# Kernel optimization log

Measured on AMD Instinct MI355X. Metric: run time of the kernel, lower is better.

Reference implementation:

```python
import math
import jax, jax.numpy as jnp
import numpy as np

NUM_HEADS = 12
NUM_LANDMARKS = 32

def iterative_inv(mat, n_iter=6):
    # mat: [B, H, m, m] row-stochastic kernel; Newton-Schulz pseudo-inverse
    m = mat.shape[-1]
    I = jnp.eye(m, dtype=mat.dtype)
    K = mat
    # 'else' branch: per-(B,H) normalization by max column sum
    denom = jnp.max(jnp.sum(K, axis=-2), axis=-1)[..., None, None]
    V = jnp.swapaxes(K, -1, -2) / denom
    for _ in range(n_iter):
        KV = jnp.matmul(K, V)
        V = jnp.matmul(0.25 * V, 13.0 * I - jnp.matmul(KV, 15.0 * I - jnp.matmul(KV, 7.0 * I - KV)))
    return V

def setup_inputs() -> dict:
    key = jax.random.key(0)
    k1, k2, k3 = jax.random.split(key, 3)
    B, N, C = 8, 2048, 768
    x = jax.random.normal(k1, (B, N, C), dtype=jnp.float32)
    w_qkv = jax.random.normal(k2, (C, 3 * C), dtype=jnp.float32) * (1.0 / math.sqrt(C))
    w_proj = jax.random.normal(k3, (C, C), dtype=jnp.float32) * (1.0 / math.sqrt(C))
    b_proj = jnp.zeros((C,), dtype=jnp.float32)
    return {"x": x, "w_qkv": w_qkv, "w_proj": w_proj, "b_proj": b_proj}

def reference(x, w_qkv, w_proj, b_proj):
    B, N, C = x.shape
    H = NUM_HEADS
    d = C // H
    m = NUM_LANDMARKS
    qkv = (x @ w_qkv).reshape(B, N, 3, H, d).transpose(2, 0, 3, 1, 4)  # [3,B,H,N,d]
    Q, K, V = qkv[0], qkv[1], qkv[2]
    scale = 1.0 / math.sqrt(math.sqrt(d))
    Q = Q * scale
    K = K * scale
    # landmark pooling: mean over contiguous chunks of size N//m
    Q_l = Q.reshape(B, H, m, N // m, d).mean(axis=-2)  # [B,H,m,d]
    K_l = K.reshape(B, H, m, N // m, d).mean(axis=-2)
    kernel_1 = jax.nn.softmax(jnp.einsum('bhnd,bhmd->bhnm', Q, K_l), axis=-1)   # [B,H,N,m]
    kernel_2 = jax.nn.softmax(jnp.einsum('bhmd,bhkd->bhmk', Q_l, K_l), axis=-1) # [B,H,m,m]
    kernel_3 = jax.nn.softmax(jnp.einsum('bhmd,bhnd->bhmn', Q_l, K), axis=-1)   # [B,H,m,N]
    X = jnp.matmul(jnp.matmul(kernel_1, iterative_inv(kernel_2)), jnp.matmul(kernel_3, V))  # [B,H,N,d]
    X = X.transpose(0, 2, 1, 3).reshape(B, N, C)
    return X @ w_proj + b_proj
```

## Files before the change

kernel.cpp:

```cpp
#include <hip/hip_runtime.h>
#include <hip/hip_bf16.h>

typedef __hip_bfloat16 bf16;
typedef __attribute__((ext_vector_type(8))) __bf16 bf16x8;
typedef __attribute__((ext_vector_type(4))) float f32x4;

#define NB 8
#define SEQ 2048
#define CH 768
#define NH 12
#define HD 64
#define NL 32
#define BHT (NB*NH)
#define TOK (NB*SEQ)
#define QK_SCALE 0.35355339059327379f

#define BAR() __builtin_amdgcn_s_barrier()
#define WLGKM0() __asm__ __volatile__("s_waitcnt lgkmcnt(0)" ::: "memory")
#define WVM(n) __asm__ __volatile__("s_waitcnt vmcnt(" #n ")" ::: "memory")

__device__ __forceinline__ void async_ld16(const bf16* g, bf16* l) {
    unsigned loff = (unsigned)__builtin_amdgcn_readfirstlane((int)(unsigned)(uintptr_t)l);
    __builtin_amdgcn_global_load_lds(
        (const __attribute__((address_space(1))) unsigned*)(uintptr_t)g,
        (__attribute__((address_space(3))) unsigned*)(uintptr_t)loff, 16, 0, 0);
}

__global__ void convert_x(const float* __restrict__ x, bf16* __restrict__ xb) {
    size_t i = ((size_t)blockIdx.x * 256 + threadIdx.x) * 8;
    float4 a = *reinterpret_cast<const float4*>(x + i);
    float4 b = *reinterpret_cast<const float4*>(x + i + 4);
    alignas(16) bf16 tmp[8];
    tmp[0] = __float2bfloat16(a.x); tmp[1] = __float2bfloat16(a.y);
    tmp[2] = __float2bfloat16(a.z); tmp[3] = __float2bfloat16(a.w);
    tmp[4] = __float2bfloat16(b.x); tmp[5] = __float2bfloat16(b.y);
    tmp[6] = __float2bfloat16(b.z); tmp[7] = __float2bfloat16(b.w);
    *reinterpret_cast<uint4*>(xb + i) = *reinterpret_cast<const uint4*>(tmp);
}

__global__ void transpose_f32(const float* __restrict__ in, bf16* __restrict__ outp,
                              int Hrows, int Wcols) {
    __shared__ float tile[32][33];
    int bx = blockIdx.x * 32, by = blockIdx.y * 32;
    int tx = threadIdx.x, ty = threadIdx.y;
    for (int i = 0; i < 32; i += 8)
        tile[ty + i][tx] = in[(size_t)(by + ty + i) * Wcols + bx + tx];
    __syncthreads();
    for (int i = 0; i < 32; i += 8)
        outp[(size_t)(bx + ty + i) * Hrows + by + tx] = __float2bfloat16(tile[tx][ty + i]);
}

template <int EPI>
__global__ __launch_bounds__(512, 2) void gemm_bt(
    const bf16* __restrict__ A, const bf16* __restrict__ Bt,
    int Nout, int Kdim,
    bf16* __restrict__ q, bf16* __restrict__ k, bf16* __restrict__ vt,
    float* __restrict__ Ql, float* __restrict__ Kl,
    float* __restrict__ outp, const float* __restrict__ bias_f) {
    __shared__ __align__(16) bf16 As[2][256 * 64];
    __shared__ __align__(16) bf16 Bs[2][192 * 64];
    const int t = threadIdx.x;
    const int wave = t >> 6, lane = t & 63;
    const int quad = lane >> 4, l15 = lane & 15;
    const int wr = wave >> 2, wc = wave & 3;

    int p = blockIdx.y * gridDim.x + blockIdx.x;
    int xcd = p & 7, j = p >> 3;
    int gx = gridDim.x;
    int bn = j % gx;
    int bm = (j / gx) * 8 + xcd;
    const int bm0 = bm * 256;
    const int bn0 = bn * 192;

    const int T = Kdim >> 6;

    const int srow = t >> 3;
    const int scol = (((t & 7) ^ (srow & 7)) << 3);
    const bf16* Abase = A + (size_t)(bm0 + srow) * Kdim + scol;
    const bf16* Bbase = Bt + (size_t)(bn0 + srow) * Kdim + scol;

    auto stA = [&](int kt, int c) {
        async_ld16(Abase + (size_t)(c * 64) * Kdim + kt * 64,
                   &As[kt & 1][c * 4096 + t * 8]);
    };
    auto stB = [&](int kt, int c) {
        async_ld16(Bbase + (size_t)(c * 64) * Kdim + kt * 64,
                   &Bs[kt & 1][c * 4096 + t * 8]);
    };

    const int swk[2] = { (quad ^ (l15 & 7)) << 3, ((4 + quad) ^ (l15 & 7)) << 3 };
    const bf16* arow = &As[0][(wr * 128 + l15) * 64];
    const bf16* brow = &Bs[0][(wc * 48 + l15) * 64];

    f32x4 acc[8][3];
    const f32x4 zero4 = {0.f, 0.f, 0.f, 0.f};
    #pragma unroll
    for (int i = 0; i < 8; i++)
        #pragma unroll
        for (int jj = 0; jj < 3; jj++) acc[i][jj] = zero4;

    stA(0, 0); stA(0, 2); stB(0, 0); stB(0, 1); stB(0, 2); stA(0, 1); stA(0, 3);
    WVM(2);
    BAR();

    bf16x8 a[4][2], b[3][2];
    #pragma unroll 2
    for (int kt = 0; kt < T; kt++) {
        const int cur = kt & 1;
        const bool nxt = (kt + 1 < T);
        const bf16* ab = arow + cur * 16384;
        const bf16* bb = brow + cur * 12288;

        #pragma unroll
        for (int mi = 0; mi < 4; mi++)
            #pragma unroll
            for (int kk = 0; kk < 2; kk++)
                a[mi][kk] = *reinterpret_cast<const bf16x8*>(ab + mi * 1024 + swk[kk]);
        #pragma unroll
        for (int ni = 0; ni < 2; ni++)
            #pragma unroll
            for (int kk = 0; kk < 2; kk++)
                b[ni][kk] = *reinterpret_cast<const bf16x8*>(bb + ni * 1024 + swk[kk]);
        if (nxt) { stA(kt + 1, 0); stA(kt + 1, 2); }
        BAR(); WLGKM0();
        __builtin_amdgcn_s_setprio(1);
        #pragma unroll
        for (int mi = 0; mi < 4; mi++)
            #pragma unroll
            for (int ni = 0; ni < 2; ni++)
                #pragma unroll
                for (int kk = 0; kk < 2; kk++)
                    acc[mi][ni] = __builtin_amdgcn_mfma_f32_16x16x32_bf16(a[mi][kk], b[ni][kk], acc[mi][ni], 0, 0, 0);
        __builtin_amdgcn_s_setprio(0);
        BAR();

        #pragma unroll
        for (int kk = 0; kk < 2; kk++)
            b[2][kk] = *reinterpret_cast<const bf16x8*>(bb + 2 * 1024 + swk[kk]);
        if (nxt) { stB(kt + 1, 0); stB(kt + 1, 1); }
        BAR(); WLGKM0();
        __builtin_amdgcn_s_setprio(1);
        #pragma unroll
        for (int mi = 0; mi < 4; mi++)
            #pragma unroll
            for (int kk = 0; kk < 2; kk++)
                acc[mi][2] = __builtin_amdgcn_mfma_f32_16x16x32_bf16(a[mi][kk], b[2][kk], acc[mi][2], 0, 0, 0);
        __builtin_amdgcn_s_setprio(0);
        if (nxt) { WVM(4); } else { WVM(0); }
        BAR();

        #pragma unroll
        for (int mi = 0; mi < 4; mi++)
            #pragma unroll
            for (int kk = 0; kk < 2; kk++)
                a[mi][kk] = *reinterpret_cast<const bf16x8*>(ab + (mi + 4) * 1024 + swk[kk]);
        if (nxt) { stB(kt + 1, 2); stA(kt + 1, 1); }
        BAR(); WLGKM0();
        __builtin_amdgcn_s_setprio(1);
        #pragma unroll
        for (int mi = 0; mi < 4; mi++)
            #pragma unroll
            for (int ni = 0; ni < 2; ni++)
                #pragma unroll
                for (int kk = 0; kk < 2; kk++)
                    acc[mi + 4][ni] = __builtin_amdgcn_mfma_f32_16x16x32_bf16(a[mi][kk], b[ni][kk], acc[mi + 4][ni], 0, 0, 0);
        __builtin_amdgcn_s_setprio(0);
        BAR();

        if (nxt) { stA(kt + 1, 3); }
        BAR();
        __builtin_amdgcn_s_setprio(1);
        #pragma unroll
        for (int mi = 0; mi < 4; mi++)
            #pragma unroll
            for (int kk = 0; kk < 2; kk++)
                acc[mi + 4][2] = __builtin_amdgcn_mfma_f32_16x16x32_bf16(a[mi][kk], b[2][kk], acc[mi + 4][2], 0, 0, 0);
        __builtin_amdgcn_s_setprio(0);
        WVM(2);
        BAR();
    }

    if (EPI == 0) {
        const int which = bn0 / CH;
        const int rem0 = bn0 - which * CH + wc * 48;
        const int b = bm0 >> 11;
        const int nnb = (bm0 & 2047) + wr * 128;
        if (which < 2) {
            bf16* dstqk = (which == 0) ? q : k;
            float* dstl = (which == 0) ? Ql : Kl;
            const int la0 = nnb >> 6;
            #pragma unroll
            for (int hf = 0; hf < 2; hf++) {
                #pragma unroll
                for (int ni = 0; ni < 3; ni++) {
                    int rem = rem0 + ni * 16;
                    int h = rem >> 6;
                    int dd = (rem & 63) + l15;
                    int bh = b * NH + h;
                    float colsum = 0.f;
                    #pragma unroll
                    for (int m2 = 0; m2 < 4; m2++) {
                        int mi = hf * 4 + m2;
                        int nn0 = nnb + mi * 16 + quad * 4;
                        #pragma unroll
                        for (int r = 0; r < 4; r++) {
                            float val = acc[mi][ni][r];
                            colsum += val;
                            dstqk[((size_t)bh * SEQ + nn0 + r) * HD + dd] = __float2bfloat16(val * QK_SCALE);
                        }
                    }
                    colsum += __shfl_xor(colsum, 16);
                    colsum += __shfl_xor(colsum, 32);
                    if (quad == 0)
                        dstl[((size_t)bh * NL + la0 + hf) * HD + dd] = colsum * (QK_SCALE / 64.f);
                }
            }
        } else {
            #pragma unroll
            for (int ni = 0; ni < 3; ni++) {
                int rem = rem0 + ni * 16;
                int h = rem >> 6;
                int dd = (rem & 63) + l15;
                int bh = b * NH + h;
                #pragma unroll
                for (int mi = 0; mi < 8; mi++) {
                    int nn0 = nnb + mi * 16 + quad * 4;
                    alignas(8) bf16 four[4];
                    #pragma unroll
                    for (int r = 0; r < 4; r++) four[r] = __float2bfloat16(acc[mi][ni][r]);
                    *reinterpret_cast<uint2*>(&vt[((size_t)bh * HD + dd) * SEQ + nn0]) =
                        *reinterpret_cast<const uint2*>(four);
                }
            }
        }
    } else {
        #pragma unroll
        for (int ni = 0; ni < 3; ni++) {
            int col = bn0 + wc * 48 + ni * 16 + l15;
            float bb = bias_f[col];
            #pragma unroll
            for (int mi = 0; mi < 8; mi++)
                #pragma unroll
                for (int r = 0; r < 4; r++) {
                    int row = bm0 + wr * 128 + mi * 16 + quad * 4 + r;
                    outp[(size_t)row * Nout + col] = acc[mi][ni][r] + bb;
                }
        }
    }
}

__device__ inline void mm32(float* Cm, const float* Am, const float* Bm, int t) {
    for (int e = t; e < 1024; e += 256) {
        int i = e >> 5, jj = e & 31;
        float s = 0.f;
        #pragma unroll
        for (int kk = 0; kk < 32; kk++) s += Am[i * 32 + kk] * Bm[kk * 32 + jj];
        Cm[e] = s;
    }
}

__global__ __launch_bounds__(256) void k3_pv(const float* __restrict__ Ql,
                                             const float* __restrict__ Klm,
                                             const bf16* __restrict__ Kb,
                                             const bf16* __restrict__ Vt,
                                             float* __restrict__ Opart,
                                             float* __restrict__ Spart,
                                             float* __restrict__ Vinv) {
    __shared__ __align__(16) char smem[69632];
    const int bh = blockIdx.x;
    const int t = threadIdx.x;

    if (blockIdx.y == 0) {
        float* K2 = (float*)smem;
        float* Vv = K2 + 1024;
        float* KV = K2 + 2048;
        float* Ta = K2 + 3072;
        float* Tb = K2 + 4096;
        float* red = K2 + 5120;
        const float* ql = Ql + (size_t)bh * NL * HD;
        const float* kl = Klm + (size_t)bh * NL * HD;

        for (int e = t; e < 1024; e += 256) {
            int i = e >> 5, jj = e & 31;
            float s = 0.f;
            #pragma unroll 8
            for (int d = 0; d < 64; d++) s += ql[i * 64 + d] * kl[jj * 64 + d];
            K2[e] = s;
        }
        __syncthreads();
        if (t < 32) {
            float mx = -1e30f;
            for (int jj = 0; jj < 32; jj++) mx = fmaxf(mx, K2[t * 32 + jj]);
            float sm = 0.f;
            for (int jj = 0; jj < 32; jj++) { float e = __expf(K2[t * 32 + jj] - mx); K2[t * 32 + jj] = e; sm += e; }
            float inv = 1.f / sm;
            for (int jj = 0; jj < 32; jj++) K2[t * 32 + jj] *= inv;
        }
        __syncthreads();
        if (t < 32) {
            float cs = 0.f;
            for (int i = 0; i < 32; i++) cs += K2[i * 32 + t];
            red[t] = cs;
        }
        __syncthreads();
        if (t == 0) {
            float mx = red[0];
            for (int jj = 1; jj < 32; jj++) mx = fmaxf(mx, red[jj]);
            red[32] = mx;
        }
        __syncthreads();
        float invden = 1.f / red[32];
        for (int e = t; e < 1024; e += 256) {
            int i = e >> 5, jj = e & 31;
            Vv[e] = K2[jj * 32 + i] * invden;
        }
        __syncthreads();
        for (int it = 0; it < 6; it++) {
            mm32(KV, K2, Vv, t);
            __syncthreads();
            for (int e = t; e < 1024; e += 256) { int i = e >> 5, jj = e & 31; Ta[e] = ((i == jj) ? 7.f : 0.f) - KV[e]; }
            __syncthreads();
            mm32(Tb, KV, Ta, t);
            __syncthreads();
            for (int e = t; e < 1024; e += 256) { int i = e >> 5, jj = e & 31; Tb[e] = ((i == jj) ? 15.f : 0.f) - Tb[e]; }
            __syncthreads();
            mm32(Ta, KV, Tb, t);
            __syncthreads();
            for (int e = t; e < 1024; e += 256) { int i = e >> 5, jj = e & 31; Ta[e] = ((i == jj) ? 13.f : 0.f) - Ta[e]; }
            __syncthreads();
            mm32(Tb, Vv, Ta, t);
            __syncthreads();
            for (int e = t; e < 1024; e += 256) Vv[e] = 0.25f * Tb[e];
            __syncthreads();
        }
        for (int e = t; e < 1024; e += 256)
            Vinv[(size_t)bh * 1024 + e] = Vv[e];
        return;
    }

    bf16* Pw0 = (bf16*)smem;
    float* Ored0 = (float*)(smem + 34816);
    float* Sred = (float*)(smem + 34816 + 33280);
    const int cc = blockIdx.y - 1;
    const int n0 = cc * 512;
    const int w = t >> 6, lane = t & 63;
    const int quad = lane >> 4, l15 = lane & 15;

    const bf16* Kbh = Kb + (size_t)bh * SEQ * HD;
    const bf16* Vtb = Vt + (size_t)bh * HD * SEQ;

    bf16x8 af[2][2];
    #pragma unroll
    for (int mt = 0; mt < 2; mt++)
        #pragma unroll
        for (int kh = 0; kh < 2; kh++) {
            const float* src = Ql + (size_t)bh * NL * HD + (mt * 16 + l15) * 64 + kh * 32 + quad * 8;
            alignas(16) bf16 tmp[8];
            #pragma unroll
            for (int jj = 0; jj < 8; jj++) tmp[jj] = __float2bfloat16(src[jj]);
            af[mt][kh] = *reinterpret_cast<const bf16x8*>(tmp);
        }

    const f32x4 zero4 = {0.f, 0.f, 0.f, 0.f};
    f32x4 oacc[2][4];
    #pragma unroll
    for (int mt = 0; mt < 2; mt++)
        #pragma unroll
        for (int nd = 0; nd < 4; nd++) oacc[mt][nd] = zero4;
    float rs[2][4];
    #pragma unroll
    for (int mt = 0; mt < 2; mt++)
        #pragma unroll
        for (int r = 0; r < 4; r++) rs[mt][r] = 0.f;

    bf16* Pme = Pw0 + w * (32 * 136);

    #pragma unroll
    for (int h = 0; h < 2; h++) {
        f32x4 sacc[2][4];
        #pragma unroll
        for (int mt = 0; mt < 2; mt++)
            #pragma unroll
            for (int nt = 0; nt < 4; nt++) sacc[mt][nt] = zero4;
        #pragma unroll
        for (int nt = 0; nt < 4; nt++) {
            int n = n0 + w * 128 + h * 64 + nt * 16 + l15;
            bf16x8 kf0 = *reinterpret_cast<const bf16x8*>(&Kbh[(size_t)n * HD + quad * 8]);
            bf16x8 kf1 = *reinterpret_cast<const bf16x8*>(&Kbh[(size_t)n * HD + 32 + quad * 8]);
            #pragma unroll
            for (int mt = 0; mt < 2; mt++) {
                sacc[mt][nt] = __builtin_amdgcn_mfma_f32_16x16x32_bf16(af[mt][0], kf0, sacc[mt][nt], 0, 0, 0);
                sacc[mt][nt] = __builtin_amdgcn_mfma_f32_16x16x32_bf16(af[mt][1], kf1, sacc[mt][nt], 0, 0, 0);
            }
        }
        #pragma unroll
        for (int mt = 0; mt < 2; mt++)
            #pragma unroll
            for (int nt = 0; nt < 4; nt++)
                #pragma unroll
                for (int r = 0; r < 4; r++) {
                    float pv = __expf(sacc[mt][nt][r]);
                    rs[mt][r] += pv;
                    int row = mt * 16 + quad * 4 + r;
                    Pme[row * 136 + h * 64 + nt * 16 + l15] = __float2bfloat16(pv);
                }
    }
    __asm__ __volatile__("s_waitcnt lgkmcnt(0)" ::: "memory");

    #pragma unroll
    for (int kt = 0; kt < 4; kt++) {
        bf16x8 pa[2];
        pa[0] = *reinterpret_cast<const bf16x8*>(&Pme[l15 * 136 + kt * 32 + quad * 8]);
        pa[1] = *reinterpret_cast<const bf16x8*>(&Pme[(16 + l15) * 136 + kt * 32 + quad * 8]);
        int kbase = n0 + w * 128 + kt * 32 + quad * 8;
        #pragma unroll
        for (int nd = 0; nd < 4; nd++) {
            bf16x8 bv = *reinterpret_cast<const bf16x8*>(&Vtb[(size_t)(nd * 16 + l15) * SEQ + kbase]);
            oacc[0][nd] = __builtin_amdgcn_mfma_f32_16x16x32_bf16(pa[0], bv, oacc[0][nd], 0, 0, 0);
            oacc[1][nd] = __builtin_amdgcn_mfma_f32_16x16x32_bf16(pa[1], bv, oacc[1][nd], 0, 0, 0);
        }
    }

    #pragma unroll
    for (int mt = 0; mt < 2; mt++)
        #pragma unroll
        for (int r = 0; r < 4; r++) {
            float v = rs[mt][r];
            #pragma unroll
            for (int o = 1; o < 16; o <<= 1) v += __shfl_xor(v, o);
            rs[mt][r] = v;
        }
    if (l15 == 0)
        #pragma unroll
        for (int mt = 0; mt < 2; mt++)
            #pragma unroll
            for (int r = 0; r < 4; r++)
                Sred[w * 32 + mt * 16 + quad * 4 + r] = rs[mt][r];
    #pragma unroll
    for (int mt = 0; mt < 2; mt++)
        #pragma unroll
        for (int nd = 0; nd < 4; nd++)
            #pragma unroll
            for (int r = 0; r < 4; r++)
                Ored0[w * (32 * 65) + (mt * 16 + quad * 4 + r) * 65 + nd * 16 + l15] = oacc[mt][nd][r];
    __syncthreads();

    float* Op = Opart + ((size_t)bh * 4 + cc) * (NL * HD);
    for (int e = t; e < 2048; e += 256) {
        int m = e >> 6, dd = e & 63;
        Op[e] = Ored0[0 * (32 * 65) + m * 65 + dd] + Ored0[1 * (32 * 65) + m * 65 + dd] +
                Ored0[2 * (32 * 65) + m * 65 + dd] + Ored0[3 * (32 * 65) + m * 65 + dd];
    }
    if (t < 32)
        Spart[((size_t)bh * 4 + cc) * NL + t] = Sred[t] + Sred[32 + t] + Sred[64 + t] + Sred[96 + t];
}

__global__ __launch_bounds__(256) void combine_w2(const float* __restrict__ Opart,
                                                  const float* __restrict__ Spart,
                                                  const float* __restrict__ Vinv,
                                                  float* __restrict__ W2) {
    __shared__ float K3[2048];
    __shared__ float Vv[1024];
    __shared__ float stot[32];
    const int bh = blockIdx.x;
    const int t = threadIdx.x;

    if (t < 32) {
        const float* sp = Spart + (size_t)bh * 4 * NL;
        stot[t] = sp[t] + sp[32 + t] + sp[64 + t] + sp[96 + t];
    }
    {
        const float* op = Opart + (size_t)bh * 4 * (NL * HD);
        for (int e = t; e < 2048; e += 256)
            K3[e] = op[e] + op[2048 + e] + op[4096 + e] + op[6144 + e];
    }
    for (int e = t; e < 1024; e += 256)
        Vv[e] = Vinv[(size_t)bh * 1024 + e];
    __syncthreads();
    for (int e = t; e < 2048; e += 256) K3[e] *= (1.f / stot[e >> 6]);
    __syncthreads();
    for (int e = t; e < 2048; e += 256) {
        int i = e >> 6, dd = e & 63;
        float s = 0.f;
        #pragma unroll
        for (int kk = 0; kk < 32; kk++) s += Vv[i * 32 + kk] * K3[kk * 64 + dd];
        W2[(size_t)bh * NL * HD + e] = s;
    }
}

__global__ __launch_bounds__(256) void rows_fused(const bf16* __restrict__ Qb,
                                                  const float* __restrict__ Kl,
                                                  const float* __restrict__ W2,
                                                  bf16* __restrict__ Xp) {
    __shared__ __align__(16) bf16 Klb[32 * 64];
    __shared__ __align__(16) bf16 W2t[64 * 32];
    __shared__ __align__(16) bf16 Pw[4][32 * 40];
    const int bh = blockIdx.x, tile = blockIdx.y;
    const int t = threadIdx.x, w = t >> 6, lane = t & 63;
    const int quad = lane >> 4, l15 = lane & 15;

    {
        const float* ksrc = Kl + (size_t)bh * NL * HD;
        const float* wsrc = W2 + (size_t)bh * NL * HD;
        int e0 = t * 8;
        #pragma unroll
        for (int jj = 0; jj < 8; jj++) {
            int e = e0 + jj;
            Klb[e] = __float2bfloat16(ksrc[e]);
            int kk = e >> 6, dd = e & 63;
            W2t[dd * 32 + kk] = __float2bfloat16(wsrc[e]);
        }
    }
    __syncthreads();

    const int b = bh / NH, h = bh - b * NH;
    const int row0 = tile * 128 + w * 32;
    const bf16* qbase = Qb + ((size_t)bh * SEQ + row0) * HD;

    const f32x4 zero4 = {0.f, 0.f, 0.f, 0.f};
    f32x4 sacc[2][2];
    #pragma unroll
    for (int mt = 0; mt < 2; mt++)
        #pragma unroll
        for (int nt = 0; nt < 2; nt++) sacc[mt][nt] = zero4;
    #pragma unroll
    for (int kh = 0; kh < 2; kh++) {
        bf16x8 bk0 = *reinterpret_cast<const bf16x8*>(&Klb[(l15) * 64 + kh * 32 + quad * 8]);
        bf16x8 bk1 = *reinterpret_cast<const bf16x8*>(&Klb[(16 + l15) * 64 + kh * 32 + quad * 8]);
        #pragma unroll
        for (int mt = 0; mt < 2; mt++) {
            bf16x8 aq = *reinterpret_cast<const bf16x8*>(&qbase[(size_t)(mt * 16 + l15) * HD + kh * 32 + quad * 8]);
            sacc[mt][0] = __builtin_amdgcn_mfma_f32_16x16x32_bf16(aq, bk0, sacc[mt][0], 0, 0, 0);
            sacc[mt][1] = __builtin_amdgcn_mfma_f32_16x16x32_bf16(aq, bk1, sacc[mt][1], 0, 0, 0);
        }
    }

    float invs[2][4];
    bf16* Pme = &Pw[w][0];
    #pragma unroll
    for (int mt = 0; mt < 2; mt++)
        #pragma unroll
        for (int r = 0; r < 4; r++) {
            float v0 = __expf(sacc[mt][0][r]);
            float v1 = __expf(sacc[mt][1][r]);
            int row = mt * 16 + quad * 4 + r;
            Pme[row * 40 + l15] = __float2bfloat16(v0);
            Pme[row * 40 + 16 + l15] = __float2bfloat16(v1);
            float v = v0 + v1;
            #pragma unroll
            for (int o = 1; o < 16; o <<= 1) v += __shfl_xor(v, o);
            invs[mt][r] = 1.f / v;
        }
    __asm__ __volatile__("s_waitcnt lgkmcnt(0)" ::: "memory");

    f32x4 oacc[2][4];
    #pragma unroll
    for (int mt = 0; mt < 2; mt++)
        #pragma unroll
        for (int nd = 0; nd < 4; nd++) oacc[mt][nd] = zero4;
    bf16x8 pa[2];
    pa[0] = *reinterpret_cast<const bf16x8*>(&Pme[l15 * 40 + quad * 8]);
    pa[1] = *reinterpret_cast<const bf16x8*>(&Pme[(16 + l15) * 40 + quad * 8]);
    #pragma unroll
    for (int nd = 0; nd < 4; nd++) {
        bf16x8 bw = *reinterpret_cast<const bf16x8*>(&W2t[(nd * 16 + l15) * 32 + quad * 8]);
        oacc[0][nd] = __builtin_amdgcn_mfma_f32_16x16x32_bf16(pa[0], bw, oacc[0][nd], 0, 0, 0);
        oacc[1][nd] = __builtin_amdgcn_mfma_f32_16x16x32_bf16(pa[1], bw, oacc[1][nd], 0, 0, 0);
    }

    #pragma unroll
    for (int mt = 0; mt < 2; mt++)
        #pragma unroll
        for (int nd = 0; nd < 4; nd++)
            #pragma unroll
            for (int r = 0; r < 4; r++) {
                int row = row0 + mt * 16 + quad * 4 + r;
                Xp[((size_t)(b * SEQ + row)) * CH + h * 64 + nd * 16 + l15] =
                    __float2bfloat16(oacc[mt][nd][r] * invs[mt][r]);
            }
}

extern "C" void kernel_launch(void* const* d_in, const int* in_sizes, int n_in,
                              void* d_out, int out_size, void* d_ws, size_t ws_size,
                              hipStream_t stream) {
    const float* x      = (const float*)d_in[0];
    const float* w_qkv  = (const float*)d_in[1];
    const float* w_proj = (const float*)d_in[2];
    const float* b_proj = (const float*)d_in[3];
    float* out = (float*)d_out;

    char* ws = (char*)d_ws;
    size_t off = 0;
    auto alloc = [&](size_t bytes) -> void* {
        void* p = ws + off;
        off += (bytes + 255) & ~(size_t)255;
        return p;
    };
    bf16* wqkvT  = (bf16*)alloc((size_t)3 * CH * CH * 2);
    bf16* wprojT = (bf16*)alloc((size_t)CH * CH * 2);
    bf16* Qb     = (bf16*)alloc((size_t)BHT * SEQ * HD * 2);
    bf16* Kb     = (bf16*)alloc((size_t)BHT * SEQ * HD * 2);
    bf16* Vt     = (bf16*)alloc((size_t)BHT * SEQ * HD * 2);
    float* Ql    = (float*)alloc((size_t)BHT * NL * HD * 4);
    float* Kl    = (float*)alloc((size_t)BHT * NL * HD * 4);
    float* Opart = (float*)alloc((size_t)BHT * 4 * NL * HD * 4);
    float* Spart = (float*)alloc((size_t)BHT * 4 * NL * 4);
    float* Vinv  = (float*)alloc((size_t)BHT * NL * NL * 4);
    float* W2    = (float*)alloc((size_t)BHT * NL * HD * 4);
    bf16* Xp     = (bf16*)alloc((size_t)TOK * CH * 2);
    if (ws_size < off) return;
    bf16* xb = Xp;

    convert_x<<<TOK * CH / 2048, 256, 0, stream>>>(x, xb);
    transpose_f32<<<dim3((3 * CH) / 32, CH / 32), dim3(32, 8), 0, stream>>>(w_qkv, wqkvT, CH, 3 * CH);
    transpose_f32<<<dim3(CH / 32, CH / 32), dim3(32, 8), 0, stream>>>(w_proj, wprojT, CH, CH);

    gemm_bt<0><<<dim3((3 * CH) / 192, TOK / 256), 512, 0, stream>>>(
        xb, wqkvT, 3 * CH, CH, Qb, Kb, Vt, Ql, Kl, nullptr, nullptr);

    k3_pv<<<dim3(BHT, 5), 256, 0, stream>>>(Ql, Kl, Kb, Vt, Opart, Spart, Vinv);
    combine_w2<<<BHT, 256, 0, stream>>>(Opart, Spart, Vinv, W2);
    rows_fused<<<dim3(BHT, SEQ / 128), 256, 0, stream>>>(Qb, Kl, W2, Xp);

    gemm_bt<1><<<dim3(CH / 192, TOK / 256), 512, 0, stream>>>(
        Xp, wprojT, CH, CH, nullptr, nullptr, nullptr, nullptr, nullptr, out, b_proj);
}
```

Baseline: 277.2 us.

## Shrink GEMM tiles to 128x192 with 4 waves and fuse prep kernels

The bf16 GEMM moves from 256x192 tiles with 8 waves to 128x192 tiles with 4 waves, each wave covering 64x96. The loads, waits and MFMA phases are reorganised into three stages per k-step. The Q/K/V and landmark epilogues are adapted so each wave writes one landmark chunk. The three preprocessing kernels (x to bf16 conversion and two weight transposes) become one launch. Smaller tiles double the grid size for better CU fill, at the cost of lower per-block operand reuse and more global/LDS traffic per FLOP.

```diff
diff --git a/kernel.cpp b/kernel.cpp
--- a/kernel.cpp
+++ b/kernel.cpp
@@ -26,23 +26,38 @@
         (__attribute__((address_space(3))) unsigned*)(uintptr_t)loff, 16, 0, 0);
 }
 
-__global__ void convert_x(const float* __restrict__ x, bf16* __restrict__ xb) {
-    size_t i = ((size_t)blockIdx.x * 256 + threadIdx.x) * 8;
-    float4 a = *reinterpret_cast<const float4*>(x + i);
-    float4 b = *reinterpret_cast<const float4*>(x + i + 4);
-    alignas(16) bf16 tmp[8];
-    tmp[0] = __float2bfloat16(a.x); tmp[1] = __float2bfloat16(a.y);
-    tmp[2] = __float2bfloat16(a.z); tmp[3] = __float2bfloat16(a.w);
-    tmp[4] = __float2bfloat16(b.x); tmp[5] = __float2bfloat16(b.y);
-    tmp[6] = __float2bfloat16(b.z); tmp[7] = __float2bfloat16(b.w);
-    *reinterpret_cast<uint4*>(xb + i) = *reinterpret_cast<const uint4*>(tmp);
-}
-
-__global__ void transpose_f32(const float* __restrict__ in, bf16* __restrict__ outp,
-                              int Hrows, int Wcols) {
+#define PREP_G0 (TOK*CH/2048)
+#define PREP_G1 ((3*CH/32)*(CH/32))
+#define PREP_G2 ((CH/32)*(CH/32))
+__global__ __launch_bounds__(256) void prep(const float* __restrict__ x, bf16* __restrict__ xb,
+                                            const float* __restrict__ w_qkv, bf16* __restrict__ wqkvT,
+                                            const float* __restrict__ w_proj, bf16* __restrict__ wprojT) {
     __shared__ float tile[32][33];
-    int bx = blockIdx.x * 32, by = blockIdx.y * 32;
-    int tx = threadIdx.x, ty = threadIdx.y;
+    const int bid = blockIdx.x;
+    const int t = threadIdx.x;
+    if (bid < PREP_G0) {
+        size_t i = ((size_t)bid * 256 + t) * 8;
+        float4 a = *reinterpret_cast<const float4*>(x + i);
+        float4 b = *reinterpret_cast<const float4*>(x + i + 4);
+        alignas(16) bf16 tmp[8];
+        tmp[0] = __float2bfloat16(a.x); tmp[1] = __float2bfloat16(a.y);
+        tmp[2] = __float2bfloat16(a.z); tmp[3] = __float2bfloat16(a.w);
+        tmp[4] = __float2bfloat16(b.x); tmp[5] = __float2bfloat16(b.y);
+        tmp[6] = __float2bfloat16(b.z); tmp[7] = __float2bfloat16(b.w);
+        *reinterpret_cast<uint4*>(xb + i) = *reinterpret_cast<const uint4*>(tmp);
+        return;
+    }
+    const float* in; bf16* outp; int Hrows, Wcols, bx, by;
+    if (bid < PREP_G0 + PREP_G1) {
+        int tb = bid - PREP_G0;
+        in = w_qkv; outp = wqkvT; Hrows = CH; Wcols = 3 * CH;
+        bx = (tb % (3 * CH / 32)) * 32; by = (tb / (3 * CH / 32)) * 32;
+    } else {
+        int tb = bid - PREP_G0 - PREP_G1;
+        in = w_proj; outp = wprojT; Hrows = CH; Wcols = CH;
+        bx = (tb % (CH / 32)) * 32; by = (tb / (CH / 32)) * 32;
+    }
+    int tx = t & 31, ty = t >> 5;
     for (int i = 0; i < 32; i += 8)
         tile[ty + i][tx] = in[(size_t)(by + ty + i) * Wcols + bx + tx];
     __syncthreads();
@@ -51,25 +66,25 @@
 }
 
 template <int EPI>
-__global__ __launch_bounds__(512, 2) void gemm_bt(
+__global__ __launch_bounds__(256, 2) void gemm_bt(
     const bf16* __restrict__ A, const bf16* __restrict__ Bt,
     int Nout, int Kdim,
     bf16* __restrict__ q, bf16* __restrict__ k, bf16* __restrict__ vt,
     float* __restrict__ Ql, float* __restrict__ Kl,
     float* __restrict__ outp, const float* __restrict__ bias_f) {
-    __shared__ __align__(16) bf16 As[2][256 * 64];
+    __shared__ __align__(16) bf16 As[2][128 * 64];
     __shared__ __align__(16) bf16 Bs[2][192 * 64];
     const int t = threadIdx.x;
     const int wave = t >> 6, lane = t & 63;
     const int quad = lane >> 4, l15 = lane & 15;
-    const int wr = wave >> 2, wc = wave & 3;
+    const int wr = wave >> 1, wc = wave & 1;
 
     int p = blockIdx.y * gridDim.x + blockIdx.x;
     int xcd = p & 7, j = p >> 3;
     int gx = gridDim.x;
     int bn = j % gx;
     int bm = (j / gx) * 8 + xcd;
-    const int bm0 = bm * 256;
+    const int bm0 = bm * 128;
     const int bn0 = bn * 192;
 
     const int T = Kdim >> 6;
@@ -80,150 +95,141 @@
     const bf16* Bbase = Bt + (size_t)(bn0 + srow) * Kdim + scol;
 
     auto stA = [&](int kt, int c) {
-        async_ld16(Abase + (size_t)(c * 64) * Kdim + kt * 64,
-                   &As[kt & 1][c * 4096 + t * 8]);
+        async_ld16(Abase + (size_t)(c * 32) * Kdim + kt * 64,
+                   &As[kt & 1][c * 2048 + t * 8]);
     };
     auto stB = [&](int kt, int c) {
-        async_ld16(Bbase + (size_t)(c * 64) * Kdim + kt * 64,
-                   &Bs[kt & 1][c * 4096 + t * 8]);
+        async_ld16(Bbase + (size_t)(c * 32) * Kdim + kt * 64,
+                   &Bs[kt & 1][c * 2048 + t * 8]);
     };
 
     const int swk[2] = { (quad ^ (l15 & 7)) << 3, ((4 + quad) ^ (l15 & 7)) << 3 };
-    const bf16* arow = &As[0][(wr * 128 + l15) * 64];
-    const bf16* brow = &Bs[0][(wc * 48 + l15) * 64];
-
-    f32x4 acc[8][3];
+    const bf16* arow = &As[0][(wr * 64 + l15) * 64];
+    const bf16* brow = &Bs[0][(wc * 96 + l15) * 64];
+
+    f32x4 acc[4][6];
     const f32x4 zero4 = {0.f, 0.f, 0.f, 0.f};
     #pragma unroll
-    for (int i = 0; i < 8; i++)
-        #pragma unroll
-        for (int jj = 0; jj < 3; jj++) acc[i][jj] = zero4;
-
-    stA(0, 0); stA(0, 2); stB(0, 0); stB(0, 1); stB(0, 2); stA(0, 1); stA(0, 3);
-    WVM(2);
+    for (int i = 0; i < 4; i++)
+        #pragma unroll
+        for (int jj = 0; jj < 6; jj++) acc[i][jj] = zero4;
+
+    stA(0, 0); stA(0, 2); stB(0, 0); stB(0, 1); stB(0, 3); stB(0, 4);
+    stB(0, 2); stB(0, 5);
+    stA(0, 1); stA(0, 3);
+    WVM(4);
     BAR();
 
-    bf16x8 a[4][2], b[3][2];
-    #pragma unroll 2
+    bf16x8 a[4][2], b[6][2];
     for (int kt = 0; kt < T; kt++) {
         const int cur = kt & 1;
         const bool nxt = (kt + 1 < T);
-        const bf16* ab = arow + cur * 16384;
+        const bf16* ab = arow + cur * 8192;
         const bf16* bb = brow + cur * 12288;
 
         #pragma unroll
-        for (int mi = 0; mi < 4; mi++)
+        for (int mi = 0; mi < 2; mi++)
             #pragma unroll
             for (int kk = 0; kk < 2; kk++)
                 a[mi][kk] = *reinterpret_cast<const bf16x8*>(ab + mi * 1024 + swk[kk]);
         #pragma unroll
-        for (int ni = 0; ni < 2; ni++)
+        for (int ni = 0; ni < 3; ni++)
             #pragma unroll
             for (int kk = 0; kk < 2; kk++)
                 b[ni][kk] = *reinterpret_cast<const bf16x8*>(bb + ni * 1024 + swk[kk]);
-        if (nxt) { stA(kt + 1, 0); stA(kt + 1, 2); }
+        if (nxt) { stA(kt + 1, 0); stA(kt + 1, 2); stB(kt + 1, 0); }
         BAR(); WLGKM0();
         __builtin_amdgcn_s_setprio(1);
         #pragma unroll
-        for (int mi = 0; mi < 4; mi++)
-            #pragma unroll
-            for (int ni = 0; ni < 2; ni++)
+        for (int mi = 0; mi < 2; mi++)
+            #pragma unroll
+            for (int ni = 0; ni < 3; ni++)
                 #pragma unroll
                 for (int kk = 0; kk < 2; kk++)
                     acc[mi][ni] = __builtin_amdgcn_mfma_f32_16x16x32_bf16(a[mi][kk], b[ni][kk], acc[mi][ni], 0, 0, 0);
         __builtin_amdgcn_s_setprio(0);
+        if (nxt) { WVM(5); } else { WVM(2); }
         BAR();
 
         #pragma unroll
-        for (int kk = 0; kk < 2; kk++)
-            b[2][kk] = *reinterpret_cast<const bf16x8*>(bb + 2 * 1024 + swk[kk]);
-        if (nxt) { stB(kt + 1, 0); stB(kt + 1, 1); }
+        for (int ni = 3; ni < 6; ni++)
+            #pragma unroll
+            for (int kk = 0; kk < 2; kk++)
+                b[ni][kk] = *reinterpret_cast<const bf16x8*>(bb + ni * 1024 + swk[kk]);
+        if (nxt) { stB(kt + 1, 1); stB(kt + 1, 3); stB(kt + 1, 4); }
         BAR(); WLGKM0();
         __builtin_amdgcn_s_setprio(1);
         #pragma unroll
-        for (int mi = 0; mi < 4; mi++)
+        for (int mi = 0; mi < 2; mi++)
+            #pragma unroll
+            for (int ni = 3; ni < 6; ni++)
+                #pragma unroll
+                for (int kk = 0; kk < 2; kk++)
+                    acc[mi][ni] = __builtin_amdgcn_mfma_f32_16x16x32_bf16(a[mi][kk], b[ni][kk], acc[mi][ni], 0, 0, 0);
+        __builtin_amdgcn_s_setprio(0);
+        if (nxt) { WVM(6); } else { WVM(0); }
+        BAR();
+
+        #pragma unroll
+        for (int mi = 2; mi < 4; mi++)
             #pragma unroll
             for (int kk = 0; kk < 2; kk++)
-                acc[mi][2] = __builtin_amdgcn_mfma_f32_16x16x32_bf16(a[mi][kk], b[2][kk], acc[mi][2], 0, 0, 0);
-        __builtin_amdgcn_s_setprio(0);
-        if (nxt) { WVM(4); } else { WVM(0); }
-        BAR();
-
-        #pragma unroll
-        for (int mi = 0; mi < 4; mi++)
-            #pragma unroll
-            for (int kk = 0; kk < 2; kk++)
-                a[mi][kk] = *reinterpret_cast<const bf16x8*>(ab + (mi + 4) * 1024 + swk[kk]);
-        if (nxt) { stB(kt + 1, 2); stA(kt + 1, 1); }
+                a[mi][kk] = *reinterpret_cast<const bf16x8*>(ab + mi * 1024 + swk[kk]);
+        if (nxt) { stB(kt + 1, 2); stB(kt + 1, 5); stA(kt + 1, 1); stA(kt + 1, 3); }
         BAR(); WLGKM0();
         __builtin_amdgcn_s_setprio(1);
         #pragma unroll
-        for (int mi = 0; mi < 4; mi++)
-            #pragma unroll
-            for (int ni = 0; ni < 2; ni++)
+        for (int mi = 2; mi < 4; mi++)
+            #pragma unroll
+            for (int ni = 0; ni < 6; ni++)
                 #pragma unroll
                 for (int kk = 0; kk < 2; kk++)
-                    acc[mi + 4][ni] = __builtin_amdgcn_mfma_f32_16x16x32_bf16(a[mi][kk], b[ni][kk], acc[mi + 4][ni], 0, 0, 0);
+                    acc[mi][ni] = __builtin_amdgcn_mfma_f32_16x16x32_bf16(a[mi][kk], b[ni][kk], acc[mi][ni], 0, 0, 0);
         __builtin_amdgcn_s_setprio(0);
-        BAR();
-
-        if (nxt) { stA(kt + 1, 3); }
-        BAR();
-        __builtin_amdgcn_s_setprio(1);
-        #pragma unroll
-        for (int mi = 0; mi < 4; mi++)
-            #pragma unroll
-            for (int kk = 0; kk < 2; kk++)
-                acc[mi + 4][2] = __builtin_amdgcn_mfma_f32_16x16x32_bf16(a[mi][kk], b[2][kk], acc[mi + 4][2], 0, 0, 0);
-        __builtin_amdgcn_s_setprio(0);
-        WVM(2);
+        if (nxt) { WVM(4); }
         BAR();
     }
 
     if (EPI == 0) {
         const int which = bn0 / CH;
-        const int rem0 = bn0 - which * CH + wc * 48;
+        const int rem0 = bn0 - which * CH + wc * 96;
         const int b = bm0 >> 11;
-        const int nnb = (bm0 & 2047) + wr * 128;
+        const int nnb = (bm0 & 2047) + wr * 64;
         if (which < 2) {
             bf16* dstqk = (which == 0) ? q : k;
             float* dstl = (which == 0) ? Ql : Kl;
-            const int la0 = nnb >> 6;
-            #pragma unroll
-            for (int hf = 0; hf < 2; hf++) {
+            const int la = nnb >> 6;
+            #pragma unroll
+            for (int ni = 0; ni < 6; ni++) {
+                int rem = rem0 + ni * 16;
+                int h = rem >> 6;
+                int dd = (rem & 63) + l15;
+                int bh = b * NH + h;
+                float colsum = 0.f;
                 #pragma unroll
-                for (int ni = 0; ni < 3; ni++) {
-                    int rem = rem0 + ni * 16;
-                    int h = rem >> 6;
-                    int dd = (rem & 63) + l15;
-                    int bh = b * NH + h;
-                    float colsum = 0.f;
+                for (int mi = 0; mi < 4; mi++) {
+                    int nn0 = nnb + mi * 16 + quad * 4;
                     #pragma unroll
-                    for (int m2 = 0; m2 < 4; m2++) {
-                        int mi = hf * 4 + m2;
-                        int nn0 = nnb + mi * 16 + quad * 4;
-                        #pragma unroll
-                        for (int r = 0; r < 4; r++) {
-                            float val = acc[mi][ni][r];
-                            colsum += val;
-                            dstqk[((size_t)bh * SEQ + nn0 + r) * HD + dd] = __float2bfloat16(val * QK_SCALE);
-                        }
+                    for (int r = 0; r < 4; r++) {
+                        float val = acc[mi][ni][r];
+                        colsum += val;
+                        dstqk[((size_t)bh * SEQ + nn0 + r) * HD + dd] = __float2bfloat16(val * QK_SCALE);
                     }
-                    colsum += __shfl_xor(colsum, 16);
-                    colsum += __shfl_xor(colsum, 32);
-                    if (quad == 0)
-                        dstl[((size_t)bh * NL + la0 + hf) * HD + dd] = colsum * (QK_SCALE / 64.f);
                 }
+                colsum += __shfl_xor(colsum, 16);
+                colsum += __shfl_xor(colsum, 32);
+                if (quad == 0)
+                    dstl[((size_t)bh * NL + la) * HD + dd] = colsum * (QK_SCALE / 64.f);
             }
         } else {
             #pragma unroll
-            for (int ni = 0; ni < 3; ni++) {
+            for (int ni = 0; ni < 6; ni++) {
                 int rem = rem0 + ni * 16;
                 int h = rem >> 6;
                 int dd = (rem & 63) + l15;
                 int bh = b * NH + h;
                 #pragma unroll
-                for (int mi = 0; mi < 8; mi++) {
+                for (int mi = 0; mi < 4; mi++) {
                     int nn0 = nnb + mi * 16 + quad * 4;
                     alignas(8) bf16 four[4];
                     #pragma unroll
@@ -235,14 +241,14 @@
         }
     } else {
         #pragma unroll
-        for (int ni = 0; ni < 3; ni++) {
-            int col = bn0 + wc * 48 + ni * 16 + l15;
+        for (int ni = 0; ni < 6; ni++) {
+            int col = bn0 + wc * 96 + ni * 16 + l15;
             float bb = bias_f[col];
             #pragma unroll
-            for (int mi = 0; mi < 8; mi++)
+            for (int mi = 0; mi < 4; mi++)
                 #pragma unroll
                 for (int r = 0; r < 4; r++) {
-                    int row = bm0 + wr * 128 + mi * 16 + quad * 4 + r;
+                    int row = bm0 + wr * 64 + mi * 16 + quad * 4 + r;
                     outp[(size_t)row * Nout + col] = acc[mi][ni][r] + bb;
                 }
         }
@@ -611,17 +617,15 @@
     if (ws_size < off) return;
     bf16* xb = Xp;
 
-    convert_x<<<TOK * CH / 2048, 256, 0, stream>>>(x, xb);
-    transpose_f32<<<dim3((3 * CH) / 32, CH / 32), dim3(32, 8), 0, stream>>>(w_qkv, wqkvT, CH, 3 * CH);
-    transpose_f32<<<dim3(CH / 32, CH / 32), dim3(32, 8), 0, stream>>>(w_proj, wprojT, CH, CH);
-
-    gemm_bt<0><<<dim3((3 * CH) / 192, TOK / 256), 512, 0, stream>>>(
+    prep<<<PREP_G0 + PREP_G1 + PREP_G2, 256, 0, stream>>>(x, xb, w_qkv, wqkvT, w_proj, wprojT);
+
+    gemm_bt<0><<<dim3((3 * CH) / 192, TOK / 128), 256, 0, stream>>>(
         xb, wqkvT, 3 * CH, CH, Qb, Kb, Vt, Ql, Kl, nullptr, nullptr);
 
     k3_pv<<<dim3(BHT, 5), 256, 0, stream>>>(Ql, Kl, Kb, Vt, Opart, Spart, Vinv);
     combine_w2<<<BHT, 256, 0, stream>>>(Opart, Spart, Vinv, W2);
     rows_fused<<<dim3(BHT, SEQ / 128), 256, 0, stream>>>(Qb, Kl, W2, Xp);
 
-    gemm_bt<1><<<dim3(CH / 192, TOK / 256), 512, 0, stream>>>(
+    gemm_bt<1><<<dim3(CH / 192, TOK / 128), 256, 0, stream>>>(
         Xp, wprojT, CH, CH, nullptr, nullptr, nullptr, nullptr, nullptr, out, b_proj);
 }
```

Measured after the change: 263.5 us. 1.05x faster.
